# Optimization experiments

Hardware: AMD Instinct MI355X
Metric: run time of the kernel (lower is better)

Reference implementation:

```python
import jax, jax.numpy as jnp
import numpy as np

BATCH, T, D_MODEL, D_STATE = 32, 4096, 256, 256
RMIN, RMAX, MAX_PHASE = 0.9, 0.999, 6.283
NEG_SLOPE = 0.01  # F.leaky_relu default


def setup_inputs() -> dict:
    key = jax.random.key(0)
    ks = jax.random.split(key, 12)
    x = jax.random.normal(ks[0], (BATCH, T, D_MODEL), jnp.float32)
    done = jnp.zeros((BATCH, T), jnp.bool_)
    h0_re = jnp.zeros((BATCH, D_STATE), jnp.float32)
    h0_im = jnp.zeros((BATCH, D_STATE), jnp.float32)
    # LRU eigenvalue init: |lambda| ~ U[rmin, rmax] (Orvieto et al.)
    u1 = jax.random.uniform(ks[1], (D_STATE,), jnp.float32)
    u2 = jax.random.uniform(ks[2], (D_STATE,), jnp.float32)
    nu_log = jnp.log(-0.5 * jnp.log(u1 * (RMAX**2 - RMIN**2) + RMIN**2))
    theta_log = jnp.log(MAX_PHASE * u2)
    lam_abs = jnp.exp(-jnp.exp(nu_log))
    gamma_log = jnp.log(jnp.sqrt(1.0 - lam_abs**2))
    sB = 1.0 / np.sqrt(2.0 * D_MODEL)
    sC = 1.0 / np.sqrt(D_STATE)
    B_re = jax.random.normal(ks[3], (D_STATE, D_MODEL), jnp.float32) * sB
    B_im = jax.random.normal(ks[4], (D_STATE, D_MODEL), jnp.float32) * sB
    C_re = jax.random.normal(ks[5], (D_STATE, D_STATE), jnp.float32) * sC
    C_im = jax.random.normal(ks[6], (D_STATE, D_STATE), jnp.float32) * sC
    D_mat = jax.random.normal(ks[7], (D_STATE, D_MODEL), jnp.float32) * (1.0 / np.sqrt(D_MODEL))
    mlp_w = jax.random.normal(ks[8], (D_MODEL, D_STATE), jnp.float32) * (1.0 / np.sqrt(D_STATE))
    mlp_b = jnp.zeros((D_MODEL,), jnp.float32)
    ln1_g = jnp.ones((D_MODEL,), jnp.float32); ln1_b = jnp.zeros((D_MODEL,), jnp.float32)
    ln2_g = jnp.ones((D_STATE,), jnp.float32); ln2_b = jnp.zeros((D_STATE,), jnp.float32)
    ln3_g = jnp.ones((D_MODEL,), jnp.float32); ln3_b = jnp.zeros((D_MODEL,), jnp.float32)
    return dict(x=x, done=done, h0_re=h0_re, h0_im=h0_im, nu_log=nu_log,
                theta_log=theta_log, gamma_log=gamma_log, B_re=B_re, B_im=B_im,
                C_re=C_re, C_im=C_im, D_mat=D_mat, mlp_w=mlp_w, mlp_b=mlp_b,
                ln1_g=ln1_g, ln1_b=ln1_b, ln2_g=ln2_g, ln2_b=ln2_b,
                ln3_g=ln3_g, ln3_b=ln3_b)


def _layernorm(x, g, b, eps=1e-5):
    mu = jnp.mean(x, axis=-1, keepdims=True)
    var = jnp.var(x, axis=-1, keepdims=True)
    return (x - mu) * jax.lax.rsqrt(var + eps) * g + b


def _leaky(x):
    return jnp.where(x >= 0, x, NEG_SLOPE * x)


def _forward(x, done, h0_re, h0_im, nu_log, theta_log, gamma_log, B_re, B_im,
             C_re, C_im, D_mat, mlp_w, mlp_b, ln1_g, ln1_b, ln2_g, ln2_b,
             ln3_g, ln3_b):
    z = _layernorm(x, ln1_g, ln1_b)          # [B,T,D]
    skip = z
    z = _leaky(z)
    # diagonal complex recurrence params
    lam_abs = jnp.exp(-jnp.exp(nu_log))
    theta = jnp.exp(theta_log)
    lam_re = lam_abs * jnp.cos(theta)        # [N]
    lam_im = lam_abs * jnp.sin(theta)
    gamma = jnp.exp(gamma_log)
    # input projection: gamma * (B z_t), complex
    u_re = jnp.einsum('btd,nd->btn', z, B_re) * gamma
    u_im = jnp.einsum('btd,nd->btn', z, B_im) * gamma
    mask = 1.0 - done.astype(z.dtype)        # [B,T], reset state where done

    def step(carry, inp):
        hr, hi = carry
        ur, ui, m = inp                       # [B,N],[B,N],[B]
        hr = hr * m[:, None]
        hi = hi * m[:, None]
        nr = lam_re * hr - lam_im * hi + ur
        ni = lam_re * hi + lam_im * hr + ui
        return (nr, ni), (nr, ni)

    xs = (jnp.swapaxes(u_re, 0, 1), jnp.swapaxes(u_im, 0, 1), jnp.swapaxes(mask, 0, 1))
    (_, _), (hs_re, hs_im) = jax.lax.scan(step, (h0_re, h0_im), xs)
    hs_re = jnp.swapaxes(hs_re, 0, 1)         # [B,T,N]
    hs_im = jnp.swapaxes(hs_im, 0, 1)
    # y = Re(C h) + D z
    y = (jnp.einsum('btn,mn->btm', hs_re, C_re)
         - jnp.einsum('btn,mn->btm', hs_im, C_im)
         + jnp.einsum('btd,nd->btn', z, D_mat))
    y = _leaky(_layernorm(y, ln2_g, ln2_b))
    y = jnp.einsum('btn,dn->btd', y, mlp_w) + mlp_b
    y = _layernorm(y, ln3_g, ln3_b)
    return y + skip


def reference(x, done, h0_re, h0_im, nu_log, theta_log, gamma_log, B_re, B_im,
              C_re, C_im, D_mat, mlp_w, mlp_b, ln1_g, ln1_b, ln2_g, ln2_b,
              ln3_g, ln3_b):
    return _forward(x, done, h0_re, h0_im, nu_log, theta_log, gamma_log,
                    B_re, B_im, C_re, C_im, D_mat, mlp_w, mlp_b,
                    ln1_g, ln1_b, ln2_g, ln2_b, ln3_g, ln3_b)
```

## Files before the change

kernel.cpp:

```cpp
#include <hip/hip_runtime.h>

#define BATCH 32
#define TLEN  4096
#define DM    256
#define NS    256
#define BT    (BATCH*TLEN)
#define CHL   64
#define NCH   (TLEN/CHL)
#define PSTRIDE ((size_t)BATCH*NCH*NS)

typedef unsigned short u16;
typedef __bf16 bf16x8 __attribute__((ext_vector_type(8)));
typedef float  f32x4  __attribute__((ext_vector_type(4)));

__device__ __forceinline__ u16 f2bf(float f) {
  unsigned u = __builtin_bit_cast(unsigned, f);
  u += 0x7FFFu + ((u >> 16) & 1u);
  return (u16)(u >> 16);
}
__device__ __forceinline__ float bf2f(u16 h) {
  unsigned u = ((unsigned)h) << 16;
  return __builtin_bit_cast(float, u);
}
__device__ __forceinline__ float wsum(float v) {
  #pragma unroll
  for (int m = 32; m >= 1; m >>= 1) v += __shfl_xor(v, m, 64);
  return v;
}
__device__ __forceinline__ void gload_lds16(const void* g, void* l) {
  __builtin_amdgcn_global_load_lds(
      (const __attribute__((address_space(1))) void*)(uintptr_t)g,
      (__attribute__((address_space(3))) void*)(unsigned)(uintptr_t)l,
      16, 0, 0);
}
#define VMCNT(N)  asm volatile("s_waitcnt vmcnt(" #N ")" ::: "memory")
#define LGKM0()   asm volatile("s_waitcnt lgkmcnt(0)" ::: "memory")
#define BARRIER() do { __builtin_amdgcn_s_barrier(); asm volatile("" ::: "memory"); } while (0)

__global__ void k_prep(const float* __restrict__ nu_log, const float* __restrict__ th_log,
                       const float* __restrict__ ga_log,
                       const float* __restrict__ B_re, const float* __restrict__ B_im,
                       const float* __restrict__ C_re, const float* __restrict__ C_im,
                       const float* __restrict__ D_mat, const float* __restrict__ mlp_w,
                       float* __restrict__ lam_re, float* __restrict__ lam_im,
                       u16* __restrict__ WB, u16* __restrict__ W2, u16* __restrict__ WM)
{
  const int tid = blockIdx.x * blockDim.x + threadIdx.x;
  const int nt  = gridDim.x * blockDim.x;
  for (int i = tid; i < NS; i += nt) {
    float la = expf(-expf(nu_log[i]));
    float th = expf(th_log[i]);
    lam_re[i] = la * cosf(th);
    lam_im[i] = la * sinf(th);
  }
  for (int i = tid; i < 512 * DM; i += nt) {
    int n = i >> 8, d = i & 255;
    float v = (n < 256) ? B_re[n * DM + d] * expf(ga_log[n])
                        : B_im[(n - 256) * DM + d] * expf(ga_log[n - 256]);
    WB[i] = f2bf(v);
  }
  for (int i = tid; i < 256 * 768; i += nt) {
    int n = i / 768, k = i - n * 768;
    float v;
    if (k < 256)      v =  C_re[n * 256 + k];
    else if (k < 512) v = -C_im[n * 256 + (k - 256)];
    else              v =  D_mat[n * 256 + (k - 512)];
    W2[i] = f2bf(v);
  }
  for (int i = tid; i < 256 * 256; i += nt) WM[i] = f2bf(mlp_w[i]);
}

__global__ __launch_bounds__(256) void k_ln1(const float* __restrict__ x,
                                             const float* __restrict__ g, const float* __restrict__ b,
                                             u16* __restrict__ za)
{
  const size_t row = (size_t)blockIdx.x * 4 + (threadIdx.x >> 6);
  const int lane = threadIdx.x & 63;
  float4 v = ((const float4*)(x + row * DM))[lane];
  float s = wsum(v.x + v.y + v.z + v.w);
  float q = wsum(v.x * v.x + v.y * v.y + v.z * v.z + v.w * v.w);
  float mean = s * (1.f / DM);
  float rstd = rsqrtf(q * (1.f / DM) - mean * mean + 1e-5f);
  float4 gg = ((const float4*)g)[lane];
  float4 bb = ((const float4*)b)[lane];
  float z0 = (v.x - mean) * rstd * gg.x + bb.x;
  float z1 = (v.y - mean) * rstd * gg.y + bb.y;
  float z2 = (v.z - mean) * rstd * gg.z + bb.z;
  float z3 = (v.w - mean) * rstd * gg.w + bb.w;
  ushort4 zl;
  zl.x = f2bf(z0 >= 0.f ? z0 : 0.01f * z0);
  zl.y = f2bf(z1 >= 0.f ? z1 : 0.01f * z1);
  zl.z = f2bf(z2 >= 0.f ? z2 : 0.01f * z2);
  zl.w = f2bf(z3 >= 0.f ? z3 : 0.01f * z3);
  ((ushort4*)(za + row * DM))[lane] = zl;
}

template <int EPI>
__global__ __launch_bounds__(512, 2) void gemm_fused(
    const u16* __restrict__ A0, int lda0, int ksplit,
    const u16* __restrict__ A1, int lda1,
    int K, const u16* __restrict__ W, int ldw,
    const float* __restrict__ g, const float* __restrict__ b,
    const float* __restrict__ bias, const u16* __restrict__ zsrc,
    u16* __restrict__ outb, float* __restrict__ outf, int ldo,
    const unsigned char* __restrict__ done,
    const float* __restrict__ lamr, const float* __restrict__ lami,
    float* __restrict__ Ebase_r, float* __restrict__ Ebase_i,
    float* __restrict__ Apr, float* __restrict__ Api)
{
  __shared__ __align__(16) u16 As[2][256 * 64];
  __shared__ __align__(16) u16 Bs[2][256 * 64];
  int mt, nw0;
  if constexpr (EPI == 0) {
    const int bid = blockIdx.x;
    const int xcd = bid & 7, s = bid >> 3;
    mt  = xcd * 64 + (s >> 1);
    nw0 = (s & 1) << 8;
  } else { mt = blockIdx.x; nw0 = 0; }
  const int m0 = mt * 256;
  const int tid = threadIdx.x;
  const int w = tid >> 6, lane = tid & 63;
  const int wr = w >> 1, wc = w & 1;

  f32x4 acc[4][8] = {};

  auto STAGE_A = [&](int p, int k0, int half) {
    const bool second = (k0 >= ksplit);
    const u16* Asrc = second ? A1 : A0;
    const int  alda = second ? lda1 : lda0;
    const int  ak   = second ? (k0 - ksplit) : k0;
    #pragma unroll
    for (int j = 0; j < 2; ++j) {
      const int r = half * 16 + w * 2 + j;
      const int row = r * 8 + (lane >> 3);
      const int col = (((lane & 7) ^ (row & 7)) << 3);
      gload_lds16(Asrc + (size_t)(m0 + row) * alda + ak + col, &As[p][r * 512]);
    }
  };
  auto STAGE_B = [&](int p, int k0, int half) {
    #pragma unroll
    for (int j = 0; j < 2; ++j) {
      const int r = half * 16 + w * 2 + j;
      const int row = r * 8 + (lane >> 3);
      const int col = (((lane & 7) ^ (row & 7)) << 3);
      gload_lds16(W + (size_t)(nw0 + row) * ldw + k0 + col, &Bs[p][r * 512]);
    }
  };

  const int NT = K >> 6;
  STAGE_A(0, 0, 0); STAGE_A(0, 0, 1);
  STAGE_B(0, 0, 0); STAGE_B(0, 0, 1);
  if (NT > 1) { STAGE_A(1, 64, 0); STAGE_A(1, 64, 1); VMCNT(4); }
  else        { VMCNT(0); }
  BARRIER();

  const int lq = (lane >> 4) << 3;

  for (int t = 0; t < NT; ++t) {
    const int p = t & 1;
    const int pn = p ^ 1;
    bf16x8 af[4][2];
    bf16x8 bfr[2][2];

    #pragma unroll
    for (int mi = 0; mi < 4; ++mi) {
      const int ra = wr * 64 + mi * 16 + (lane & 15);
      #pragma unroll
      for (int kki = 0; kki < 2; ++kki) {
        const int koff = kki * 32 + lq;
        af[mi][kki] = *(const bf16x8*)((const char*)&As[p][0] + ra * 128 + ((koff * 2) ^ ((ra & 7) << 4)));
      }
    }
    #pragma unroll
    for (int nn = 0; nn < 2; ++nn) {
      const int rb = wc * 128 + nn * 16 + (lane & 15);
      #pragma unroll
      for (int kki = 0; kki < 2; ++kki) {
        const int koff = kki * 32 + lq;
        bfr[nn][kki] = *(const bf16x8*)((const char*)&Bs[p][0] + rb * 128 + ((koff * 2) ^ ((rb & 7) << 4)));
      }
    }
    if (t + 1 < NT) STAGE_B(pn, (t + 1) << 6, 0);
    BARRIER(); LGKM0();
    __builtin_amdgcn_s_setprio(1);
    #pragma unroll
    for (int kki = 0; kki < 2; ++kki)
      #pragma unroll
      for (int nn = 0; nn < 2; ++nn)
        #pragma unroll
        for (int mi = 0; mi < 4; ++mi)
          acc[mi][nn] = __builtin_amdgcn_mfma_f32_16x16x32_bf16(af[mi][kki], bfr[nn][kki], acc[mi][nn], 0, 0, 0);
    __builtin_amdgcn_s_setprio(0);
    BARRIER();

    #pragma unroll
    for (int q = 1; q < 4; ++q) {
      #pragma unroll
      for (int nn = 0; nn < 2; ++nn) {
        const int rb = wc * 128 + (q * 2 + nn) * 16 + (lane & 15);
        #pragma unroll
        for (int kki = 0; kki < 2; ++kki) {
          const int koff = kki * 32 + lq;
          bfr[nn][kki] = *(const bf16x8*)((const char*)&Bs[p][0] + rb * 128 + ((koff * 2) ^ ((rb & 7) << 4)));
        }
      }
      if (q == 1)      { if (t + 1 < NT) STAGE_B(pn, (t + 1) << 6, 1); }
      else if (q == 2) { if (t + 2 < NT) STAGE_A(p,  (t + 2) << 6, 0); }
      else             { if (t + 2 < NT) STAGE_A(p,  (t + 2) << 6, 1); }
      BARRIER(); LGKM0();
      __builtin_amdgcn_s_setprio(1);
      #pragma unroll
      for (int kki = 0; kki < 2; ++kki)
        #pragma unroll
        for (int nn = 0; nn < 2; ++nn)
          #pragma unroll
          for (int mi = 0; mi < 4; ++mi)
            acc[mi][q * 2 + nn] = __builtin_amdgcn_mfma_f32_16x16x32_bf16(af[mi][kki], bfr[nn][kki], acc[mi][q * 2 + nn], 0, 0, 0);
      __builtin_amdgcn_s_setprio(0);
      if (q == 3) { if (t + 2 < NT) { VMCNT(4); } else { VMCNT(0); } }
      BARRIER();
    }
  }

  const int rq = (lane >> 4) << 2;

  if constexpr (EPI == 0) {
    #pragma unroll
    for (int mi = 0; mi < 4; ++mi) {
      #pragma unroll
      for (int rr = 0; rr < 4; ++rr) {
        const int row = wr * 64 + mi * 16 + rq + rr;
        const size_t rbase = (size_t)(m0 + row) * ldo + nw0;
        #pragma unroll
        for (int ni = 0; ni < 8; ++ni) {
          const int col = wc * 128 + ni * 16 + (lane & 15);
          outb[rbase + col] = f2bf(acc[mi][ni][rr]);
        }
      }
    }
    const int hq = lane >> 4;
    const int ln = lane & 15;
    const int gchunk = (m0 >> 6) + wr;
    const int trow0 = m0 + wr * 64;
    const int part = nw0 >> 8;
    uchar4 dn[4];
    #pragma unroll
    for (int mi = 0; mi < 4; ++mi)
      dn[mi] = *(const uchar4*)(done + trow0 + mi * 16 + hq * 4);
    #pragma unroll
    for (int ni = 0; ni < 8; ++ni) {
      const int n = wc * 128 + ni * 16 + ln;
      const float lr = lamr[n], li = lami[n];
      float Ar = 1.f, Ai = 0.f, Er = 0.f, Ei = 0.f;
      #pragma unroll
      for (int mi = 0; mi < 4; ++mi) {
        float ar = 1.f, ai = 0.f, er = 0.f, ei = 0.f;
        #pragma unroll
        for (int rr = 0; rr < 4; ++rr) {
          const unsigned char db = (rr == 0) ? dn[mi].x : (rr == 1) ? dn[mi].y
                                 : (rr == 2) ? dn[mi].z : dn[mi].w;
          const float m = db ? 0.f : 1.f;
          const float uv = acc[mi][ni][rr];
          const float ur = part == 0 ? uv : 0.f;
          const float ui = part == 0 ? 0.f : uv;
          const float lmr = lr * m, lmi = li * m;
          const float na_r = lmr * ar - lmi * ai, na_i = lmr * ai + lmi * ar;
          ar = na_r; ai = na_i;
          const float ne_r = lmr * er - lmi * ei + ur;
          const float ne_i = lmr * ei + lmi * er + ui;
          er = ne_r; ei = ne_i;
        }
        #pragma unroll
        for (int d = 1; d <= 2; d <<= 1) {
          int sl = lane - 16 * d; sl = sl < 0 ? lane : sl;
          const float pa_r = __shfl(ar, sl, 64), pa_i = __shfl(ai, sl, 64);
          const float pe_r = __shfl(er, sl, 64), pe_i = __shfl(ei, sl, 64);
          if (hq >= d) {
            const float ca_r = ar * pa_r - ai * pa_i, ca_i = ar * pa_i + ai * pa_r;
            const float ce_r = er + (ar * pe_r - ai * pe_i);
            const float ce_i = ei + (ar * pe_i + ai * pe_r);
            ar = ca_r; ai = ca_i; er = ce_r; ei = ce_i;
          }
        }
        ar = __shfl(ar, ln + 48, 64); ai = __shfl(ai, ln + 48, 64);
        er = __shfl(er, ln + 48, 64); ei = __shfl(ei, ln + 48, 64);
        const float nA_r = ar * Ar - ai * Ai, nA_i = ar * Ai + ai * Ar;
        const float nE_r = er + (ar * Er - ai * Ei);
        const float nE_i = ei + (ar * Ei + ai * Er);
        Ar = nA_r; Ai = nA_i; Er = nE_r; Ei = nE_i;
      }
      if (hq == 0) {
        const size_t idx = (size_t)gchunk * 256 + n;
        Ebase_r[(size_t)part * PSTRIDE + idx] = Er;
        Ebase_i[(size_t)part * PSTRIDE + idx] = Ei;
        if (part == 0) { Apr[idx] = Ar; Api[idx] = Ai; }
      }
    }
    return;
  }

  float g8[8], b8[8], bias8[8];
  #pragma unroll
  for (int ni = 0; ni < 8; ++ni) {
    const int col = wc * 128 + ni * 16 + (lane & 15);
    g8[ni] = g[col]; b8[ni] = b[col];
    if constexpr (EPI == 2) bias8[ni] = bias[col];
  }

  float* red = (float*)&As[0][0];
  #pragma unroll
  for (int mi = 0; mi < 4; ++mi) {
    #pragma unroll
    for (int rr = 0; rr < 4; ++rr) {
      float s = 0.f, q = 0.f;
      #pragma unroll
      for (int ni = 0; ni < 8; ++ni) {
        float v = acc[mi][ni][rr];
        if constexpr (EPI == 2) v += bias8[ni];
        s += v; q += v * v;
      }
      #pragma unroll
      for (int mm = 1; mm < 16; mm <<= 1) {
        s += __shfl_xor(s, mm, 64);
        q += __shfl_xor(q, mm, 64);
      }
      if ((lane & 15) == 0) {
        const int row = wr * 64 + mi * 16 + rq + rr;
        red[row * 4 + wc * 2]     = s;
        red[row * 4 + wc * 2 + 1] = q;
      }
    }
  }
  __syncthreads();

  #pragma unroll
  for (int mi = 0; mi < 4; ++mi) {
    #pragma unroll
    for (int rr = 0; rr < 4; ++rr) {
      const int row = wr * 64 + mi * 16 + rq + rr;
      const float S = red[row * 4] + red[row * 4 + 2];
      const float Q = red[row * 4 + 1] + red[row * 4 + 3];
      const float mean = S * (1.f / 256.f);
      const float rstd = rsqrtf(Q * (1.f / 256.f) - mean * mean + 1e-5f);
      const size_t rbase = (size_t)(m0 + row) * 256;
      #pragma unroll
      for (int ni = 0; ni < 8; ++ni) {
        const int col = wc * 128 + ni * 16 + (lane & 15);
        float v = acc[mi][ni][rr];
        if constexpr (EPI == 2) v += bias8[ni];
        float t = (v - mean) * rstd * g8[ni] + b8[ni];
        if constexpr (EPI == 1) {
          t = t >= 0.f ? t : 0.01f * t;
          outb[rbase + col] = f2bf(t);
        } else {
          float zv = bf2f(zsrc[rbase + col]);
          zv = zv >= 0.f ? zv : 100.f * zv;
          outf[rbase + col] = t + zv;
        }
      }
    }
  }
}

__global__ __launch_bounds__(256) void scan_comb(const float* __restrict__ h0re,
    const float* __restrict__ h0im,
    const float* __restrict__ Apr, const float* __restrict__ Api,
    const float* __restrict__ Er, const float* __restrict__ Ei,
    float* __restrict__ Sre, float* __restrict__ Sim)
{
  const int b = blockIdx.x, n = threadIdx.x;
  float sre = h0re[b * NS + n], sim = h0im[b * NS + n];
  for (int c = 0; c < NCH; ++c) {
    const size_t idx = ((size_t)(b * NCH + c)) * NS + n;
    Sre[idx] = sre; Sim[idx] = sim;
    const float ar = Apr[idx], ai = Api[idx];
    const float er = Er[idx] + Er[PSTRIDE + idx];
    const float ei = Ei[idx] + Ei[PSTRIDE + idx];
    const float nr = ar * sre - ai * sim + er;
    const float ni = ar * sim + ai * sre + ei;
    sre = nr; sim = ni;
  }
}

__global__ __launch_bounds__(256) void scan_passC(u16* __restrict__ u,
    const unsigned char* __restrict__ done,
    const float* __restrict__ lam_re, const float* __restrict__ lam_im,
    const float* __restrict__ Sre, const float* __restrict__ Sim)
{
  const int b = blockIdx.x / NCH, c = blockIdx.x % NCH;
  const int n = threadIdx.x;
  const float lr = lam_re[n], li = lam_im[n];
  const size_t sidx = ((size_t)(b * NCH + c)) * NS + n;
  float hre = Sre[sidx], him = Sim[sidx];
  const int t0 = c * CHL;
  for (int t = t0; t < t0 + CHL; ++t) {
    const float m = done[b * TLEN + t] ? 0.f : 1.f;
    const float hr = hre * m, hi = him * m;
    const size_t base = ((size_t)(b * TLEN + t)) * 512;
    const float ur = bf2f(u[base + n]), ui = bf2f(u[base + 256 + n]);
    hre = lr * hr - li * hi + ur;
    him = lr * hi + li * hr + ui;
    u[base + n]       = f2bf(hre);
    u[base + 256 + n] = f2bf(him);
  }
}

extern "C" void kernel_launch(void* const* d_in, const int* in_sizes, int n_in,
                              void* d_out, int out_size, void* d_ws, size_t ws_size,
                              hipStream_t stream)
{
  const float* x      = (const float*)d_in[0];
  const unsigned char* done = (const unsigned char*)d_in[1];
  const float* h0re   = (const float*)d_in[2];
  const float* h0im   = (const float*)d_in[3];
  const float* nu_log = (const float*)d_in[4];
  const float* th_log = (const float*)d_in[5];
  const float* ga_log = (const float*)d_in[6];
  const float* B_re   = (const float*)d_in[7];
  const float* B_im   = (const float*)d_in[8];
  const float* C_re   = (const float*)d_in[9];
  const float* C_im   = (const float*)d_in[10];
  const float* D_mat  = (const float*)d_in[11];
  const float* mlp_w  = (const float*)d_in[12];
  const float* mlp_b  = (const float*)d_in[13];
  const float* ln1_g  = (const float*)d_in[14];
  const float* ln1_b  = (const float*)d_in[15];
  const float* ln2_g  = (const float*)d_in[16];
  const float* ln2_b  = (const float*)d_in[17];
  const float* ln3_g  = (const float*)d_in[18];
  const float* ln3_b  = (const float*)d_in[19];
  (void)in_sizes; (void)n_in; (void)out_size; (void)ws_size;

  char* ws = (char*)d_ws;
  float* lam_re = (float*)(ws + 0);
  float* lam_im = (float*)(ws + 1024);
  u16* WB = (u16*)(ws + 4096);
  u16* W2 = (u16*)(ws + 4096 + 512 * 256 * 2);
  u16* WM = (u16*)(ws + 4096 + 512 * 256 * 2 + 256 * 768 * 2);

  size_t off = (size_t)1 << 20;
  u16* za    = (u16*)(ws + off); off += (size_t)BT * DM * 2;
  u16* ubuf  = (u16*)(ws + off); off += (size_t)BT * 512 * 2;
  u16* ybuf  = (u16*)(ws + off); off += (size_t)BT * NS * 2;
  float* Apr = (float*)(ws + off); off += PSTRIDE * 4;
  float* Api = (float*)(ws + off); off += PSTRIDE * 4;
  float* Er  = (float*)(ws + off); off += PSTRIDE * 4 * 2;
  float* Ei  = (float*)(ws + off); off += PSTRIDE * 4 * 2;
  float* Sre = (float*)(ws + off); off += PSTRIDE * 4;
  float* Sim = (float*)(ws + off); off += PSTRIDE * 4;

  k_prep<<<256, 256, 0, stream>>>(nu_log, th_log, ga_log, B_re, B_im, C_re, C_im,
                                  D_mat, mlp_w, lam_re, lam_im, WB, W2, WM);
  k_ln1<<<BT / 4, 256, 0, stream>>>(x, ln1_g, ln1_b, za);
  gemm_fused<0><<<1024, 512, 0, stream>>>(za, 256, 1 << 28, nullptr, 0,
                                          256, WB, 256, nullptr, nullptr,
                                          nullptr, nullptr, ubuf, nullptr, 512,
                                          done, lam_re, lam_im, Er, Ei, Apr, Api);
  scan_comb<<<BATCH, 256, 0, stream>>>(h0re, h0im, Apr, Api, Er, Ei, Sre, Sim);
  scan_passC<<<BATCH * NCH, 256, 0, stream>>>(ubuf, done, lam_re, lam_im, Sre, Sim);
  gemm_fused<1><<<BT / 256, 512, 0, stream>>>(ubuf, 512, 512, za, 256,
                                              768, W2, 768, ln2_g, ln2_b,
                                              nullptr, nullptr, ybuf, nullptr, 256,
                                              nullptr, nullptr, nullptr,
                                              nullptr, nullptr, nullptr, nullptr);
  gemm_fused<2><<<BT / 256, 512, 0, stream>>>(ybuf, 256, 256, ybuf, 256,
                                              256, WM, 256, ln3_g, ln3_b,
                                              mlp_b, za, nullptr, (float*)d_out, 256,
                                              nullptr, nullptr, nullptr,
                                              nullptr, nullptr, nullptr, nullptr);
}
```

Before: 367.9 us.

## Split u-GEMM into dedicated kernel with sequential per-column chunk scan epilogue

Moves the first projection GEMM into its own specialised kernel with fixed K and strides. The epilogue changes: it no longer does an in-register shuffle-based parallel scan over the accumulators. It writes u to global memory, syncs, then has each thread run a sequential 64-step recurrence per (chunk, state) column, reading back the bf16 values it just stored. When no done flag is set in a chunk, the decay product is computed in closed form as lambda^64 by repeated squaring, which drops half the complex multiplies. This trades shuffle and register pressure for strided global re-reads and a serial dependency chain. It also changes numerics slightly, because the scan now reads bf16-rounded u instead of fp32 accumulators.

```diff
diff --git a/kernel.cpp b/kernel.cpp
--- a/kernel.cpp
+++ b/kernel.cpp
@@ -95,28 +95,20 @@
   ((ushort4*)(za + row * DM))[lane] = zl;
 }
 
-template <int EPI>
-__global__ __launch_bounds__(512, 2) void gemm_fused(
-    const u16* __restrict__ A0, int lda0, int ksplit,
-    const u16* __restrict__ A1, int lda1,
-    int K, const u16* __restrict__ W, int ldw,
-    const float* __restrict__ g, const float* __restrict__ b,
-    const float* __restrict__ bias, const u16* __restrict__ zsrc,
-    u16* __restrict__ outb, float* __restrict__ outf, int ldo,
+__global__ __launch_bounds__(512, 2) void gemm_u4(
+    const u16* __restrict__ A0, const u16* __restrict__ W,
+    u16* __restrict__ outb,
     const unsigned char* __restrict__ done,
     const float* __restrict__ lamr, const float* __restrict__ lami,
-    float* __restrict__ Ebase_r, float* __restrict__ Ebase_i,
+    float* __restrict__ Epr, float* __restrict__ Epi,
     float* __restrict__ Apr, float* __restrict__ Api)
 {
   __shared__ __align__(16) u16 As[2][256 * 64];
   __shared__ __align__(16) u16 Bs[2][256 * 64];
-  int mt, nw0;
-  if constexpr (EPI == 0) {
-    const int bid = blockIdx.x;
-    const int xcd = bid & 7, s = bid >> 3;
-    mt  = xcd * 64 + (s >> 1);
-    nw0 = (s & 1) << 8;
-  } else { mt = blockIdx.x; nw0 = 0; }
+  const int bid = blockIdx.x;
+  const int xcd = bid & 7, sl = bid >> 3;
+  const int mt  = xcd * 64 + (sl >> 1);
+  const int nw0 = (sl & 1) << 8;
   const int m0 = mt * 256;
   const int tid = threadIdx.x;
   const int w = tid >> 6, lane = tid & 63;
@@ -125,16 +117,12 @@
   f32x4 acc[4][8] = {};
 
   auto STAGE_A = [&](int p, int k0, int half) {
-    const bool second = (k0 >= ksplit);
-    const u16* Asrc = second ? A1 : A0;
-    const int  alda = second ? lda1 : lda0;
-    const int  ak   = second ? (k0 - ksplit) : k0;
     #pragma unroll
     for (int j = 0; j < 2; ++j) {
       const int r = half * 16 + w * 2 + j;
       const int row = r * 8 + (lane >> 3);
       const int col = (((lane & 7) ^ (row & 7)) << 3);
-      gload_lds16(Asrc + (size_t)(m0 + row) * alda + ak + col, &As[p][r * 512]);
+      gload_lds16(A0 + (size_t)(m0 + row) * 256 + k0 + col, &As[p][r * 512]);
     }
   };
   auto STAGE_B = [&](int p, int k0, int half) {
@@ -143,15 +131,14 @@
       const int r = half * 16 + w * 2 + j;
       const int row = r * 8 + (lane >> 3);
       const int col = (((lane & 7) ^ (row & 7)) << 3);
-      gload_lds16(W + (size_t)(nw0 + row) * ldw + k0 + col, &Bs[p][r * 512]);
+      gload_lds16(W + (size_t)(nw0 + row) * 256 + k0 + col, &Bs[p][r * 512]);
     }
   };
 
-  const int NT = K >> 6;
+  const int NT = 4;
   STAGE_A(0, 0, 0); STAGE_A(0, 0, 1);
   STAGE_B(0, 0, 0); STAGE_B(0, 0, 1);
-  if (NT > 1) { STAGE_A(1, 64, 0); STAGE_A(1, 64, 1); VMCNT(4); }
-  else        { VMCNT(0); }
+  STAGE_A(1, 64, 0); STAGE_A(1, 64, 1); VMCNT(4);
   BARRIER();
 
   const int lq = (lane >> 4) << 3;
@@ -223,81 +210,181 @@
   }
 
   const int rq = (lane >> 4) << 2;
-
-  if constexpr (EPI == 0) {
+  #pragma unroll
+  for (int mi = 0; mi < 4; ++mi) {
+    #pragma unroll
+    for (int rr = 0; rr < 4; ++rr) {
+      const int row = wr * 64 + mi * 16 + rq + rr;
+      const size_t rbase = (size_t)(m0 + row) * 512 + nw0;
+      #pragma unroll
+      for (int ni = 0; ni < 8; ++ni) {
+        const int col = wc * 128 + ni * 16 + (lane & 15);
+        outb[rbase + col] = f2bf(acc[mi][ni][rr]);
+      }
+    }
+  }
+  __syncthreads();
+
+  const int part = nw0 >> 8;
+  for (int task = tid; task < 1024; task += 512) {
+    const int c = task >> 8;
+    const int n = task & 255;
+    const float lr = lamr[n], li = lami[n];
+    const unsigned char* dptr = done + (size_t)(m0 + c * 64);
+    unsigned any = 0;
+    #pragma unroll
+    for (int j = 0; j < 16; ++j) any |= ((const unsigned*)dptr)[j];
+    const u16* ucol = outb + (size_t)(m0 + c * 64) * 512 + nw0 + n;
+    float Er_ = 0.f, Ei_ = 0.f, Ar_, Ai_;
+    if (any == 0) {
+      #pragma unroll 8
+      for (int s = 0; s < 64; ++s) {
+        const float uv = bf2f(ucol[(size_t)s * 512]);
+        const float ner = lr * Er_ - li * Ei_ + (part == 0 ? uv : 0.f);
+        const float nei = lr * Ei_ + li * Er_ + (part == 0 ? 0.f : uv);
+        Er_ = ner; Ei_ = nei;
+      }
+      float pr = lr, pi = li;
+      #pragma unroll
+      for (int sq = 0; sq < 6; ++sq) { float a = pr * pr - pi * pi; float bq = 2.f * pr * pi; pr = a; pi = bq; }
+      Ar_ = pr; Ai_ = pi;
+    } else {
+      Ar_ = 1.f; Ai_ = 0.f;
+      for (int s = 0; s < 64; ++s) {
+        const float m = dptr[s] ? 0.f : 1.f;
+        const float uv = bf2f(ucol[(size_t)s * 512]);
+        const float lmr = lr * m, lmi = li * m;
+        const float nar = lmr * Ar_ - lmi * Ai_, nai = lmr * Ai_ + lmi * Ar_;
+        Ar_ = nar; Ai_ = nai;
+        const float ner = lmr * Er_ - lmi * Ei_ + (part == 0 ? uv : 0.f);
+        const float nei = lmr * Ei_ + lmi * Er_ + (part == 0 ? 0.f : uv);
+        Er_ = ner; Ei_ = nei;
+      }
+    }
+    const size_t idx = (size_t)(mt * 4 + c) * 256 + n;
+    Epr[(size_t)part * PSTRIDE + idx] = Er_;
+    Epi[(size_t)part * PSTRIDE + idx] = Ei_;
+    if (part == 0) { Apr[idx] = Ar_; Api[idx] = Ai_; }
+  }
+}
+
+template <int EPI>
+__global__ __launch_bounds__(512, 2) void gemm_fused(
+    const u16* __restrict__ A0, int lda0, int ksplit,
+    const u16* __restrict__ A1, int lda1,
+    int K, const u16* __restrict__ W, int ldw,
+    const float* __restrict__ g, const float* __restrict__ b,
+    const float* __restrict__ bias, const u16* __restrict__ zsrc,
+    u16* __restrict__ outb, float* __restrict__ outf)
+{
+  __shared__ __align__(16) u16 As[2][256 * 64];
+  __shared__ __align__(16) u16 Bs[2][256 * 64];
+  const int m0 = blockIdx.x * 256;
+  const int tid = threadIdx.x;
+  const int w = tid >> 6, lane = tid & 63;
+  const int wr = w >> 1, wc = w & 1;
+
+  f32x4 acc[4][8] = {};
+
+  auto STAGE_A = [&](int p, int k0, int half) {
+    const bool second = (k0 >= ksplit);
+    const u16* Asrc = second ? A1 : A0;
+    const int  alda = second ? lda1 : lda0;
+    const int  ak   = second ? (k0 - ksplit) : k0;
+    #pragma unroll
+    for (int j = 0; j < 2; ++j) {
+      const int r = half * 16 + w * 2 + j;
+      const int row = r * 8 + (lane >> 3);
+      const int col = (((lane & 7) ^ (row & 7)) << 3);
+      gload_lds16(Asrc + (size_t)(m0 + row) * alda + ak + col, &As[p][r * 512]);
+    }
+  };
+  auto STAGE_B = [&](int p, int k0, int half) {
+    #pragma unroll
+    for (int j = 0; j < 2; ++j) {
+      const int r = half * 16 + w * 2 + j;
+      const int row = r * 8 + (lane >> 3);
+      const int col = (((lane & 7) ^ (row & 7)) << 3);
+      gload_lds16(W + (size_t)row * ldw + k0 + col, &Bs[p][r * 512]);
+    }
+  };
+
+  const int NT = K >> 6;
+  STAGE_A(0, 0, 0); STAGE_A(0, 0, 1);
+  STAGE_B(0, 0, 0); STAGE_B(0, 0, 1);
+  if (NT > 1) { STAGE_A(1, 64, 0); STAGE_A(1, 64, 1); VMCNT(4); }
+  else        { VMCNT(0); }
+  BARRIER();
+
+  const int lq = (lane >> 4) << 3;
+
+  for (int t = 0; t < NT; ++t) {
+    const int p = t & 1;
+    const int pn = p ^ 1;
+    bf16x8 af[4][2];
+    bf16x8 bfr[2][2];
+
     #pragma unroll
     for (int mi = 0; mi < 4; ++mi) {
-      #pragma unroll
-      for (int rr = 0; rr < 4; ++rr) {
-        const int row = wr * 64 + mi * 16 + rq + rr;
-        const size_t rbase = (size_t)(m0 + row) * ldo + nw0;
+      const int ra = wr * 64 + mi * 16 + (lane & 15);
+      #pragma unroll
+      for (int kki = 0; kki < 2; ++kki) {
+        const int koff = kki * 32 + lq;
+        af[mi][kki] = *(const bf16x8*)((const char*)&As[p][0] + ra * 128 + ((koff * 2) ^ ((ra & 7) << 4)));
+      }
+    }
+    #pragma unroll
+    for (int nn = 0; nn < 2; ++nn) {
+      const int rb = wc * 128 + nn * 16 + (lane & 15);
+      #pragma unroll
+      for (int kki = 0; kki < 2; ++kki) {
+        const int koff = kki * 32 + lq;
+        bfr[nn][kki] = *(const bf16x8*)((const char*)&Bs[p][0] + rb * 128 + ((koff * 2) ^ ((rb & 7) << 4)));
+      }
+    }
+    if (t + 1 < NT) STAGE_B(pn, (t + 1) << 6, 0);
+    BARRIER(); LGKM0();
+    __builtin_amdgcn_s_setprio(1);
+    #pragma unroll
+    for (int kki = 0; kki < 2; ++kki)
+      #pragma unroll
+      for (int nn = 0; nn < 2; ++nn)
         #pragma unroll
-        for (int ni = 0; ni < 8; ++ni) {
-          const int col = wc * 128 + ni * 16 + (lane & 15);
-          outb[rbase + col] = f2bf(acc[mi][ni][rr]);
+        for (int mi = 0; mi < 4; ++mi)
+          acc[mi][nn] = __builtin_amdgcn_mfma_f32_16x16x32_bf16(af[mi][kki], bfr[nn][kki], acc[mi][nn], 0, 0, 0);
+    __builtin_amdgcn_s_setprio(0);
+    BARRIER();
+
+    #pragma unroll
+    for (int q = 1; q < 4; ++q) {
+      #pragma unroll
+      for (int nn = 0; nn < 2; ++nn) {
+        const int rb = wc * 128 + (q * 2 + nn) * 16 + (lane & 15);
+        #pragma unroll
+        for (int kki = 0; kki < 2; ++kki) {
+          const int koff = kki * 32 + lq;
+          bfr[nn][kki] = *(const bf16x8*)((const char*)&Bs[p][0] + rb * 128 + ((koff * 2) ^ ((rb & 7) << 4)));
         }
       }
-    }
-    const int hq = lane >> 4;
-    const int ln = lane & 15;
-    const int gchunk = (m0 >> 6) + wr;
-    const int trow0 = m0 + wr * 64;
-    const int part = nw0 >> 8;
-    uchar4 dn[4];
-    #pragma unroll
-    for (int mi = 0; mi < 4; ++mi)
-      dn[mi] = *(const uchar4*)(done + trow0 + mi * 16 + hq * 4);
-    #pragma unroll
-    for (int ni = 0; ni < 8; ++ni) {
-      const int n = wc * 128 + ni * 16 + ln;
-      const float lr = lamr[n], li = lami[n];
-      float Ar = 1.f, Ai = 0.f, Er = 0.f, Ei = 0.f;
-      #pragma unroll
-      for (int mi = 0; mi < 4; ++mi) {
-        float ar = 1.f, ai = 0.f, er = 0.f, ei = 0.f;
+      if (q == 1)      { if (t + 1 < NT) STAGE_B(pn, (t + 1) << 6, 1); }
+      else if (q == 2) { if (t + 2 < NT) STAGE_A(p,  (t + 2) << 6, 0); }
+      else             { if (t + 2 < NT) STAGE_A(p,  (t + 2) << 6, 1); }
+      BARRIER(); LGKM0();
+      __builtin_amdgcn_s_setprio(1);
+      #pragma unroll
+      for (int kki = 0; kki < 2; ++kki)
         #pragma unroll
-        for (int rr = 0; rr < 4; ++rr) {
-          const unsigned char db = (rr == 0) ? dn[mi].x : (rr == 1) ? dn[mi].y
-                                 : (rr == 2) ? dn[mi].z : dn[mi].w;
-          const float m = db ? 0.f : 1.f;
-          const float uv = acc[mi][ni][rr];
-          const float ur = part == 0 ? uv : 0.f;
-          const float ui = part == 0 ? 0.f : uv;
-          const float lmr = lr * m, lmi = li * m;
-          const float na_r = lmr * ar - lmi * ai, na_i = lmr * ai + lmi * ar;
-          ar = na_r; ai = na_i;
-          const float ne_r = lmr * er - lmi * ei + ur;
-          const float ne_i = lmr * ei + lmi * er + ui;
-          er = ne_r; ei = ne_i;
-        }
-        #pragma unroll
-        for (int d = 1; d <= 2; d <<= 1) {
-          int sl = lane - 16 * d; sl = sl < 0 ? lane : sl;
-          const float pa_r = __shfl(ar, sl, 64), pa_i = __shfl(ai, sl, 64);
-          const float pe_r = __shfl(er, sl, 64), pe_i = __shfl(ei, sl, 64);
-          if (hq >= d) {
-            const float ca_r = ar * pa_r - ai * pa_i, ca_i = ar * pa_i + ai * pa_r;
-            const float ce_r = er + (ar * pe_r - ai * pe_i);
-            const float ce_i = ei + (ar * pe_i + ai * pe_r);
-            ar = ca_r; ai = ca_i; er = ce_r; ei = ce_i;
-          }
-        }
-        ar = __shfl(ar, ln + 48, 64); ai = __shfl(ai, ln + 48, 64);
-        er = __shfl(er, ln + 48, 64); ei = __shfl(ei, ln + 48, 64);
-        const float nA_r = ar * Ar - ai * Ai, nA_i = ar * Ai + ai * Ar;
-        const float nE_r = er + (ar * Er - ai * Ei);
-        const float nE_i = ei + (ar * Ei + ai * Er);
-        Ar = nA_r; Ai = nA_i; Er = nE_r; Ei = nE_i;
-      }
-      if (hq == 0) {
-        const size_t idx = (size_t)gchunk * 256 + n;
-        Ebase_r[(size_t)part * PSTRIDE + idx] = Er;
-        Ebase_i[(size_t)part * PSTRIDE + idx] = Ei;
-        if (part == 0) { Apr[idx] = Ar; Api[idx] = Ai; }
-      }
-    }
-    return;
-  }
+        for (int nn = 0; nn < 2; ++nn)
+          #pragma unroll
+          for (int mi = 0; mi < 4; ++mi)
+            acc[mi][q * 2 + nn] = __builtin_amdgcn_mfma_f32_16x16x32_bf16(af[mi][kki], bfr[nn][kki], acc[mi][q * 2 + nn], 0, 0, 0);
+      __builtin_amdgcn_s_setprio(0);
+      if (q == 3) { if (t + 2 < NT) { VMCNT(4); } else { VMCNT(0); } }
+      BARRIER();
+    }
+  }
+
+  const int rq = (lane >> 4) << 2;
 
   float g8[8], b8[8], bias8[8];
   #pragma unroll
@@ -452,20 +539,14 @@
   k_prep<<<256, 256, 0, stream>>>(nu_log, th_log, ga_log, B_re, B_im, C_re, C_im,
                                   D_mat, mlp_w, lam_re, lam_im, WB, W2, WM);
   k_ln1<<<BT / 4, 256, 0, stream>>>(x, ln1_g, ln1_b, za);
-  gemm_fused<0><<<1024, 512, 0, stream>>>(za, 256, 1 << 28, nullptr, 0,
-                                          256, WB, 256, nullptr, nullptr,
-                                          nullptr, nullptr, ubuf, nullptr, 512,
-                                          done, lam_re, lam_im, Er, Ei, Apr, Api);
+  gemm_u4<<<1024, 512, 0, stream>>>(za, WB, ubuf, done, lam_re, lam_im,
+                                    Er, Ei, Apr, Api);
   scan_comb<<<BATCH, 256, 0, stream>>>(h0re, h0im, Apr, Api, Er, Ei, Sre, Sim);
   scan_passC<<<BATCH * NCH, 256, 0, stream>>>(ubuf, done, lam_re, lam_im, Sre, Sim);
   gemm_fused<1><<<BT / 256, 512, 0, stream>>>(ubuf, 512, 512, za, 256,
                                               768, W2, 768, ln2_g, ln2_b,
-                                              nullptr, nullptr, ybuf, nullptr, 256,
-                                              nullptr, nullptr, nullptr,
-                                              nullptr, nullptr, nullptr, nullptr);
+                                              nullptr, nullptr, ybuf, nullptr);
   gemm_fused<2><<<BT / 256, 512, 0, stream>>>(ybuf, 256, 256, ybuf, 256,
                                               256, WM, 256, ln3_g, ln3_b,
-                                              mlp_b, za, nullptr, (float*)d_out, 256,
-                                              nullptr, nullptr, nullptr,
-                                              nullptr, nullptr, nullptr, nullptr);
-}
+                                              mlp_b, za, nullptr, (float*)d_out);
+}
```

New measurement: 344.2 us. -6.4%, faster.
